# Kernel optimization log

Hardware: AMD Instinct MI355X
Metric: run time of the kernel (lower is better)

## Reference

```python
import math
import jax, jax.numpy as jnp
import numpy as np

EPS = 1e-5
TEMP = 1.0
ROPE_BASE = 10000.0


def _ln(x, g, b):
    m = x.mean(-1, keepdims=True)
    v = ((x - m) ** 2).mean(-1, keepdims=True)
    return (x - m) / jnp.sqrt(v + EPS) * g + b


def _trigrams(n_heads):
    # 8 trigrams = all sign patterns of {-1,+1}^3, L2-normalized rows
    bits = ((np.arange(8)[:, None] >> np.arange(3)[None, :]) & 1).astype(np.float32)
    t = bits * 2.0 - 1.0
    t = t / np.linalg.norm(t, axis=1, keepdims=True)
    return jnp.asarray(t[:n_heads])  # [H, 3]


def _rope_tables(T, D):
    inv = 1.0 / (ROPE_BASE ** (np.arange(0, D, 2, dtype=np.float32) / D))
    ang = np.arange(T, dtype=np.float32)[:, None] * inv[None, :]  # [T, D/2]
    cos = np.concatenate([np.cos(ang), np.cos(ang)], axis=1)  # [T, D]
    sin = np.concatenate([np.sin(ang), np.sin(ang)], axis=1)
    return jnp.asarray(cos), jnp.asarray(sin)


def _apply_rope(x, cos, sin):
    # x: [B, H, T, D], rotate-half convention
    d = x.shape[-1] // 2
    rot = jnp.concatenate([-x[..., d:], x[..., :d]], axis=-1)
    return x * cos + rot * sin


def setup_inputs() -> dict:
    key = jax.random.key(0)
    ks = jax.random.split(key, 8)
    B, T, C, H = 2, 2048, 1024, 8
    FFN, QD = 4096, 6
    w = 0.02
    return {
        "x": jax.random.normal(ks[0], (B, T, C), jnp.float32),
        "ln_attn_g": jnp.ones((C,), jnp.float32),
        "ln_attn_b": jnp.zeros((C,), jnp.float32),
        "qkv_w": jax.random.normal(ks[1], (3 * C, C), jnp.float32) * w,
        "out_w": jax.random.normal(ks[2], (C, C), jnp.float32) * w,
        "head_scales": jax.random.normal(ks[3], (H,), jnp.float32) * 0.1,
        "ln_hex_g": jnp.ones((C,), jnp.float32),
        "ln_hex_b": jnp.zeros((C,), jnp.float32),
        "to_qd_w": jax.random.normal(ks[4], (QD, C), jnp.float32) * w,
        "from_qd_w": jax.random.normal(ks[5], (C, QD), jnp.float32) * w,
        "hex_scale": jnp.ones((1,), jnp.float32),
        "ln_ffn_g": jnp.ones((C,), jnp.float32),
        "ln_ffn_b": jnp.zeros((C,), jnp.float32),
        "ffn_w1": jax.random.normal(ks[6], (FFN, C), jnp.float32) * w,
        "ffn_b1": jnp.zeros((FFN,), jnp.float32),
        "ffn_w2": jax.random.normal(ks[7], (C, FFN), jnp.float32) * w,
        "ffn_b2": jnp.zeros((C,), jnp.float32),
    }


def _layer(x, ln_attn_g, ln_attn_b, qkv_w, out_w, head_scales,
           ln_hex_g, ln_hex_b, to_qd_w, from_qd_w, hex_scale,
           ln_ffn_g, ln_ffn_b, ffn_w1, ffn_b1, ffn_w2, ffn_b2):
    B, T, C = x.shape
    H = head_scales.shape[0]
    D = C // H

    # ---- attention with trigram geo-bias ----
    h = _ln(x, ln_attn_g, ln_attn_b)
    qkv = (h @ qkv_w.T).reshape(B, T, 3, H, D).transpose(2, 0, 3, 1, 4)
    q, k, v = qkv[0], qkv[1], qkv[2]  # [B, H, T, D]
    cos, sin = _rope_tables(T, D)
    q = _apply_rope(q, cos, sin)
    k = _apply_rope(k, cos, sin)

    mask = jnp.tril(jnp.ones((T, T), bool))
    scale = jnp.float32(1.0 / math.sqrt(D))
    scores = jnp.einsum('bhtd,bhsd->bhts', q, k) * scale
    scores = jnp.where(mask, scores, -jnp.inf)
    attn = jax.nn.softmax(scores, axis=-1)
    out = attn @ v  # [B, H, T, D]

    # rank-1 geometric correction (flash path)
    dirs = _trigrams(H)  # [H, 3]
    qp = jnp.einsum('bhtd,hd->bht', q[..., :3], dirs)
    kp = jnp.einsum('bhtd,hd->bht', k[..., :3], dirs)
    geo = qp[..., :, None] * kp[..., None, :]  # [B, H, T, T]
    geo_attn = jax.nn.softmax(jnp.where(mask, geo, -jnp.inf), axis=-1)
    geo_out = geo_attn @ v
    out = out + head_scales[None, :, None, None] * jax.lax.stop_gradient(geo_out - out)

    out = out.transpose(0, 2, 1, 3).reshape(B, T, C) @ out_w.T
    x = x + out

    # ---- hexagram VQ (factored6: per-dim binary quantize w/ straight-through) ----
    h = _ln(x, ln_hex_g, ln_hex_b)
    zq = h @ to_qd_w.T  # [B, T, 6]
    soft = jnp.tanh(zq / TEMP)
    hard = jnp.where(zq >= 0, 1.0, -1.0).astype(zq.dtype)
    zq_out = soft + jax.lax.stop_gradient(hard - soft)
    x = x + hex_scale[0] * (zq_out @ from_qd_w.T)

    # ---- FFN (GELU) ----
    h = _ln(x, ln_ffn_g, ln_ffn_b)
    x = x + (jax.nn.gelu(h @ ffn_w1.T + ffn_b1, approximate=False) @ ffn_w2.T + ffn_b2)
    return x


def reference(x, ln_attn_g, ln_attn_b, qkv_w, out_w, head_scales,
              ln_hex_g, ln_hex_b, to_qd_w, from_qd_w, hex_scale,
              ln_ffn_g, ln_ffn_b, ffn_w1, ffn_b1, ffn_w2, ffn_b2):
    return _layer(x, ln_attn_g, ln_attn_b, qkv_w, out_w, head_scales,
                  ln_hex_g, ln_hex_b, to_qd_w, from_qd_w, hex_scale,
                  ln_ffn_g, ln_ffn_b, ffn_w1, ffn_b1, ffn_w2, ffn_b2)
```

## Files before the change

kernel.cpp:

```cpp
#include <hip/hip_runtime.h>
#include <hip/hip_bf16.h>

typedef __attribute__((ext_vector_type(4))) float f32x4;
typedef __attribute__((ext_vector_type(8))) short short8;
typedef __attribute__((ext_vector_type(4))) short short4v;

namespace {

constexpr int Tt = 2048, Cc = 1024, Hh = 8, Dd = 128, FFNd = 4096;
constexpr int Bb = 2;
constexpr int Mrows = Bb * Tt;
constexpr float kNEG = -1e30f;
constexpr float L2E = 1.4426950408889634f;

static __device__ __forceinline__ float b2f(unsigned short u) {
  return __uint_as_float(((unsigned int)u) << 16);
}
static __device__ __forceinline__ unsigned short f2b(float f) {
  __hip_bfloat16 h = __float2bfloat16(f);
  unsigned short u;
  __builtin_memcpy(&u, &h, 2);
  return u;
}
static __device__ __forceinline__ void split2(float v, unsigned short& h, unsigned short& l) {
  h = f2b(v);
  float r = v - b2f(h);
  l = f2b(r);
}
static __device__ __forceinline__ void split3(float v, unsigned short& h, unsigned short& m,
                                              unsigned short& l) {
  h = f2b(v);
  float r = v - b2f(h);
  m = f2b(r);
  float r2 = r - b2f(m);
  l = f2b(r2);
}
static __device__ __forceinline__ float wave_sum(float v) {
#pragma unroll
  for (int m = 1; m < 64; m <<= 1) v += __shfl_xor(v, m);
  return v;
}

__global__ __launch_bounds__(256) void cast_kernel(const float* __restrict__ in,
                                                   unsigned short* __restrict__ out, int n) {
  int i = (blockIdx.x * 256 + threadIdx.x) * 4;
  if (i + 3 < n) {
    float4 v = *(const float4*)&in[i];
    short4v o;
    o.x = (short)f2b(v.x); o.y = (short)f2b(v.y); o.z = (short)f2b(v.z); o.w = (short)f2b(v.w);
    *(short4v*)&out[i] = o;
  }
}
__global__ __launch_bounds__(256) void wsplit2_k(const float* __restrict__ in,
                                                 unsigned short* __restrict__ o0,
                                                 unsigned short* __restrict__ o1, int n) {
  int i = (blockIdx.x * 256 + threadIdx.x) * 4;
  if (i + 3 < n) {
    float4 v = *(const float4*)&in[i];
    short4v a, b;
#pragma unroll
    for (int j = 0; j < 4; ++j) {
      unsigned short hh, ll;
      split2(((float*)&v)[j], hh, ll);
      a[j] = (short)hh; b[j] = (short)ll;
    }
    *(short4v*)&o0[i] = a;
    *(short4v*)&o1[i] = b;
  }
}
__global__ __launch_bounds__(256) void wsplit3_k(const float* __restrict__ in,
                                                 unsigned short* __restrict__ o0,
                                                 unsigned short* __restrict__ o1,
                                                 unsigned short* __restrict__ o2, int n) {
  int i = (blockIdx.x * 256 + threadIdx.x) * 4;
  if (i + 3 < n) {
    float4 v = *(const float4*)&in[i];
    short4v a, b, c;
#pragma unroll
    for (int j = 0; j < 4; ++j) {
      unsigned short hh, mm, ll;
      split3(((float*)&v)[j], hh, mm, ll);
      a[j] = (short)hh; b[j] = (short)mm; c[j] = (short)ll;
    }
    *(short4v*)&o0[i] = a;
    *(short4v*)&o1[i] = b;
    *(short4v*)&o2[i] = c;
  }
}

__global__ __launch_bounds__(256) void ln_split(const float* __restrict__ x,
                                                const float* __restrict__ g,
                                                const float* __restrict__ bb,
                                                unsigned short* __restrict__ oh,
                                                unsigned short* __restrict__ ol) {
  int row = blockIdx.x * 4 + (threadIdx.x >> 6);
  int lane = threadIdx.x & 63;
  const float* xr = x + (size_t)row * Cc;
  float v[16];
  float s = 0.f;
#pragma unroll
  for (int c = 0; c < 4; ++c) {
    float4 t = *(const float4*)&xr[c * 256 + lane * 4];
    v[c * 4 + 0] = t.x; v[c * 4 + 1] = t.y; v[c * 4 + 2] = t.z; v[c * 4 + 3] = t.w;
    s += t.x + t.y + t.z + t.w;
  }
  s = wave_sum(s);
  float mean = s * (1.f / Cc);
  float s2 = 0.f;
#pragma unroll
  for (int j = 0; j < 16; ++j) { float d = v[j] - mean; s2 += d * d; }
  s2 = wave_sum(s2);
  float rstd = 1.0f / sqrtf(s2 * (1.f / Cc) + 1e-5f);
#pragma unroll
  for (int c = 0; c < 4; ++c) {
    short4v a, b;
#pragma unroll
    for (int j = 0; j < 4; ++j) {
      int idx = c * 256 + lane * 4 + j;
      float hv = (v[c * 4 + j] - mean) * rstd * g[idx] + bb[idx];
      unsigned short hh, ll;
      split2(hv, hh, ll);
      a[j] = (short)hh; b[j] = (short)ll;
    }
    *(short4v*)&oh[(size_t)row * Cc + c * 256 + lane * 4] = a;
    *(short4v*)&ol[(size_t)row * Cc + c * 256 + lane * 4] = b;
  }
}

template <int NS, int EPI>
__global__ __launch_bounds__(256) void gemm_pn(
    const unsigned short* __restrict__ A0, const unsigned short* __restrict__ A1,
    const unsigned short* __restrict__ A2, const unsigned short* __restrict__ W0,
    const unsigned short* __restrict__ W1, const unsigned short* __restrict__ W2,
    unsigned short* __restrict__ outP, size_t planeStride, float* __restrict__ outF,
    const float* __restrict__ resid, int Nn, int Kk) {
  __shared__ __align__(16) unsigned short As[NS][128 * 32];
  __shared__ __align__(16) unsigned short Bs[NS][128 * 32];
  int m0 = blockIdx.x * 128, n0 = blockIdx.y * 128;
  int tid = threadIdx.x, lane = tid & 63, wid = tid >> 6;
  int wr = (wid >> 1) * 64, wc = (wid & 1) * 64;
  int g = lane >> 4, r16 = lane & 15;
  const unsigned short* Aps[3] = {A0, A1, A2};
  const unsigned short* Wps[3] = {W0, W1, W2};
  f32x4 acc[4][4];
#pragma unroll
  for (int mi = 0; mi < 4; ++mi)
#pragma unroll
    for (int ni = 0; ni < 4; ++ni) acc[mi][ni] = (f32x4){0.f, 0.f, 0.f, 0.f};
  for (int k0 = 0; k0 < Kk; k0 += 32) {
    __syncthreads();
#pragma unroll
    for (int s = 0; s < NS; ++s)
#pragma unroll
      for (int it = 0; it < 2; ++it) {
        int slot = it * 256 + tid;
        int row = slot >> 2, sw = slot & 3;
        int cc = sw ^ (row & 3);
        *(short8*)&As[s][slot * 8] = *(const short8*)&Aps[s][(size_t)(m0 + row) * Kk + k0 + cc * 8];
        *(short8*)&Bs[s][slot * 8] = *(const short8*)&Wps[s][(size_t)(n0 + row) * Kk + k0 + cc * 8];
      }
    __syncthreads();
    short8 af[NS][4], bfv[NS][4];
#pragma unroll
    for (int mi = 0; mi < 4; ++mi) {
      int row = wr + mi * 16 + r16;
      int so = row * 32 + ((g ^ (row & 3)) * 8);
#pragma unroll
      for (int s = 0; s < NS; ++s) af[s][mi] = *(short8*)&As[s][so];
    }
#pragma unroll
    for (int ni = 0; ni < 4; ++ni) {
      int row = wc + ni * 16 + r16;
      int so = row * 32 + ((g ^ (row & 3)) * 8);
#pragma unroll
      for (int s = 0; s < NS; ++s) bfv[s][ni] = *(short8*)&Bs[s][so];
    }
    __builtin_amdgcn_s_setprio(1);
#pragma unroll
    for (int mi = 0; mi < 4; ++mi)
#pragma unroll
      for (int ni = 0; ni < 4; ++ni) {
        f32x4 a = acc[mi][ni];
        if constexpr (NS == 3) {
          a = __builtin_amdgcn_mfma_f32_16x16x32_bf16(af[1][mi], bfv[1][ni], a, 0, 0, 0);
          a = __builtin_amdgcn_mfma_f32_16x16x32_bf16(af[0][mi], bfv[2][ni], a, 0, 0, 0);
          a = __builtin_amdgcn_mfma_f32_16x16x32_bf16(af[2][mi], bfv[0][ni], a, 0, 0, 0);
        }
        a = __builtin_amdgcn_mfma_f32_16x16x32_bf16(af[0][mi], bfv[1][ni], a, 0, 0, 0);
        a = __builtin_amdgcn_mfma_f32_16x16x32_bf16(af[1][mi], bfv[0][ni], a, 0, 0, 0);
        a = __builtin_amdgcn_mfma_f32_16x16x32_bf16(af[0][mi], bfv[0][ni], a, 0, 0, 0);
        acc[mi][ni] = a;
      }
    __builtin_amdgcn_s_setprio(0);
  }
#pragma unroll
  for (int mi = 0; mi < 4; ++mi)
#pragma unroll
    for (int ni = 0; ni < 4; ++ni)
#pragma unroll
      for (int r = 0; r < 4; ++r) {
        int row = m0 + wr + mi * 16 + 4 * g + r;
        int col = n0 + wc + ni * 16 + r16;
        float v = acc[mi][ni][r];
        if constexpr (EPI == 0) {
          int sec = col >> 10, cw = col & 1023;
          unsigned short hh, ll;
          split2(v, hh, ll);
          outP[(size_t)(2 * sec) * planeStride + (size_t)row * Cc + cw] = hh;
          outP[(size_t)(2 * sec + 1) * planeStride + (size_t)row * Cc + cw] = ll;
        } else {
          size_t o = (size_t)row * Nn + col;
          outF[o] = v + resid[o];
        }
      }
}

template <int EPI>
__global__ __launch_bounds__(256) void gemm_bt(const unsigned short* __restrict__ A,
                                               const unsigned short* __restrict__ W,
                                               float* __restrict__ outF,
                                               unsigned short* __restrict__ outB,
                                               const float* __restrict__ bias,
                                               const float* __restrict__ resid, int Nn, int Kk) {
  __shared__ __align__(16) unsigned short As[128 * 32];
  __shared__ __align__(16) unsigned short Bs[128 * 32];
  int m0 = blockIdx.x * 128, n0 = blockIdx.y * 128;
  int tid = threadIdx.x, lane = tid & 63, wid = tid >> 6;
  int wr = (wid >> 1) * 64, wc = (wid & 1) * 64;
  int g = lane >> 4, r16 = lane & 15;
  f32x4 acc[4][4];
#pragma unroll
  for (int mi = 0; mi < 4; ++mi)
#pragma unroll
    for (int ni = 0; ni < 4; ++ni) acc[mi][ni] = (f32x4){0.f, 0.f, 0.f, 0.f};
  for (int k0 = 0; k0 < Kk; k0 += 32) {
    __syncthreads();
#pragma unroll
    for (int c = 0; c < 2; ++c) {
      int chunk = tid + c * 256;
      int row = chunk >> 2, cc = chunk & 3;
      int sw = cc ^ (row & 3);
      *(short8*)&As[row * 32 + sw * 8] = *(const short8*)&A[(size_t)(m0 + row) * Kk + k0 + cc * 8];
      *(short8*)&Bs[row * 32 + sw * 8] = *(const short8*)&W[(size_t)(n0 + row) * Kk + k0 + cc * 8];
    }
    __syncthreads();
    short8 af[4], bfr[4];
#pragma unroll
    for (int mi = 0; mi < 4; ++mi) {
      int row = wr + mi * 16 + r16;
      af[mi] = *(short8*)&As[row * 32 + ((g ^ (row & 3)) * 8)];
    }
#pragma unroll
    for (int ni = 0; ni < 4; ++ni) {
      int row = wc + ni * 16 + r16;
      bfr[ni] = *(short8*)&Bs[row * 32 + ((g ^ (row & 3)) * 8)];
    }
    __builtin_amdgcn_s_setprio(1);
#pragma unroll
    for (int mi = 0; mi < 4; ++mi)
#pragma unroll
      for (int ni = 0; ni < 4; ++ni)
        acc[mi][ni] = __builtin_amdgcn_mfma_f32_16x16x32_bf16(af[mi], bfr[ni], acc[mi][ni], 0, 0, 0);
    __builtin_amdgcn_s_setprio(0);
  }
#pragma unroll
  for (int mi = 0; mi < 4; ++mi)
#pragma unroll
    for (int ni = 0; ni < 4; ++ni)
#pragma unroll
      for (int r = 0; r < 4; ++r) {
        int row = m0 + wr + mi * 16 + 4 * g + r;
        int col = n0 + wc + ni * 16 + r16;
        size_t o = (size_t)row * Nn + col;
        float v = acc[mi][ni][r];
        if constexpr (EPI == 2) {
          v += bias[col];
          v = 0.5f * v * (1.f + erff(v * 0.70710678118654752f));
          outB[o] = f2b(v);
        } else {
          v += bias[col];
          outF[o] = v + resid[o];
        }
      }
}

__global__ __launch_bounds__(256) void rope_table(float* __restrict__ ct, float* __restrict__ st) {
  int idx = blockIdx.x * 256 + threadIdx.x;
  int t = idx >> 6, i = idx & 63;
  float e = (float)i * (1.f / 64.f);
  float p = powf(10000.0f, e);
  float inv = 1.0f / p;
  float ang = (float)t * inv;
  ct[idx] = cosf(ang);
  st[idx] = sinf(ang);
}

__global__ __launch_bounds__(256) void rope_apply(unsigned short* __restrict__ qh_p,
                                                  unsigned short* __restrict__ ql_p,
                                                  const unsigned short* __restrict__ kh_p,
                                                  const unsigned short* __restrict__ kl_p,
                                                  unsigned short* __restrict__ khsw,
                                                  unsigned short* __restrict__ klsw,
                                                  const float* __restrict__ ct,
                                                  const float* __restrict__ st,
                                                  float* __restrict__ qp, float* __restrict__ kp) {
  int w = blockIdx.x * 4 + (threadIdx.x >> 6);
  int lane = threadIdx.x & 63;
  int b = w / (Hh * Tt);
  int rem = w % (Hh * Tt);
  int h = rem / Tt;
  int t = rem % Tt;
  size_t base = (size_t)(b * Tt + t) * Cc + h * Dd;
  float cv = ct[t * 64 + lane], sv = st[t * 64 + lane];
  float q_lo = b2f(qh_p[base + lane]) + b2f(ql_p[base + lane]);
  float q_hi = b2f(qh_p[base + lane + 64]) + b2f(ql_p[base + lane + 64]);
  float qn_lo = q_lo * cv - q_hi * sv;
  float qn_hi = q_hi * cv + q_lo * sv;
  unsigned short hh, ll;
  split2(qn_lo, hh, ll);
  qh_p[base + lane] = hh; ql_p[base + lane] = ll;
  split2(qn_hi, hh, ll);
  qh_p[base + lane + 64] = hh; ql_p[base + lane + 64] = ll;
  float k_lo = b2f(kh_p[base + lane]) + b2f(kl_p[base + lane]);
  float k_hi = b2f(kh_p[base + lane + 64]) + b2f(kl_p[base + lane + 64]);
  float kn_lo = k_lo * cv - k_hi * sv;
  float kn_hi = k_hi * cv + k_lo * sv;
  size_t krow = ((size_t)(b * Hh + h) * Tt + t) * 128;
  int tsw = t & 7;
  int d0 = lane, d1 = lane + 64;
  int c0 = (((d0 >> 3) ^ tsw) << 3) | (d0 & 7);
  int c1 = (((d1 >> 3) ^ tsw) << 3) | (d1 & 7);
  split2(kn_lo, hh, ll);
  khsw[krow + c0] = hh; klsw[krow + c0] = ll;
  split2(kn_hi, hh, ll);
  khsw[krow + c1] = hh; klsw[krow + c1] = ll;
  float t0 = (((h >> 0) & 1) ? 1.f : -1.f) * 0.57735026918962576f;
  float t1 = (((h >> 1) & 1) ? 1.f : -1.f) * 0.57735026918962576f;
  float t2 = (((h >> 2) & 1) ? 1.f : -1.f) * 0.57735026918962576f;
  float q0v = __shfl(qn_lo, 0), q1v = __shfl(qn_lo, 1), q2v = __shfl(qn_lo, 2);
  float k0v = __shfl(kn_lo, 0), k1v = __shfl(kn_lo, 1), k2v = __shfl(kn_lo, 2);
  if (lane == 0) {
    qp[(size_t)(b * Hh + h) * Tt + t] = q0v * t0 + q1v * t1 + q2v * t2;
    kp[(size_t)(b * Hh + h) * Tt + t] = k0v * t0 + k1v * t1 + k2v * t2;
  }
}

__global__ __launch_bounds__(256) void vtrans(const unsigned short* __restrict__ vh_p,
                                              const unsigned short* __restrict__ vl_p,
                                              unsigned short* __restrict__ vth,
                                              unsigned short* __restrict__ vtl) {
  __shared__ unsigned short Lh[64 * 68], Ll[64 * 68];
  int bidx = blockIdx.x;
  int dd = bidx & 1;
  int tt = (bidx >> 1) & 31;
  int bh = bidx >> 6;
  int b = bh >> 3, h = bh & 7;
  int tid = threadIdx.x;
#pragma unroll
  for (int it = 0; it < 2; ++it) {
    int chunk = tid + it * 256;
    int tr = chunk >> 3, c8 = chunk & 7;
    size_t src = (size_t)(b * Tt + tt * 64 + tr) * Cc + h * Dd + dd * 64 + c8 * 8;
    short8 vh = *(const short8*)&vh_p[src];
    short8 vl = *(const short8*)&vl_p[src];
    *(short4v*)&Lh[tr * 68 + c8 * 8] = *(short4v*)&vh;
    *(short4v*)&Lh[tr * 68 + c8 * 8 + 4] = *((short4v*)&vh + 1);
    *(short4v*)&Ll[tr * 68 + c8 * 8] = *(short4v*)&vl;
    *(short4v*)&Ll[tr * 68 + c8 * 8 + 4] = *((short4v*)&vl + 1);
  }
  __syncthreads();
#pragma unroll
  for (int it = 0; it < 2; ++it) {
    int chunk = tid + it * 256;
    int dr = chunk >> 3, t8 = chunk & 7;
    short8 oh, ol;
#pragma unroll
    for (int e = 0; e < 8; ++e) {
      oh[e] = (short)Lh[(t8 * 8 + e) * 68 + dr];
      ol[e] = (short)Ll[(t8 * 8 + e) * 68 + dr];
    }
    size_t dst = (size_t)(bh * Dd + dd * 64 + dr) * Tt + tt * 64 + t8 * 8;
    *(short8*)&vth[dst] = oh;
    *(short8*)&vtl[dst] = ol;
  }
}

__global__ __launch_bounds__(256, 2) void attn_v3(
    const unsigned short* __restrict__ qh_p, const unsigned short* __restrict__ ql_p,
    const unsigned short* __restrict__ khsw, const unsigned short* __restrict__ klsw,
    const unsigned short* __restrict__ vth, const unsigned short* __restrict__ vtl,
    const float* __restrict__ qp, const float* __restrict__ kp,
    const float* __restrict__ head_scales, unsigned short* __restrict__ ao0,
    unsigned short* __restrict__ ao1, unsigned short* __restrict__ ao2) {
  int cix = blockIdx.x & 255, rix = blockIdx.x >> 8;
  int bh = cix >> 4, ii = cix & 15;
  int qblk = rix ? ii : 31 - ii;
  int b = bh >> 3, h = bh & 7;
  int q0 = qblk * 64;
  int tid = threadIdx.x, lane = tid & 63, wid = tid >> 6;
  int wq0 = q0 + wid * 16;
  int g = lane >> 4, r16 = lane & 15;
  __shared__ __align__(16) unsigned short Ksh[32 * 128], Ksl[32 * 128];
  __shared__ __align__(16) unsigned short Vsh[128 * 34], Vsl[128 * 34];

  short8 qfh[4], qfl[4];
#pragma unroll
  for (int c4 = 0; c4 < 4; ++c4) {
    size_t qoff = (size_t)(b * Tt + wq0 + r16) * Cc + h * Dd + c4 * 32 + g * 8;
    qfh[c4] = *(const short8*)&qh_p[qoff];
    qfl[c4] = *(const short8*)&ql_p[qoff];
  }
  float hs = head_scales[h];
  const float* kpb = kp + (size_t)bh * Tt;
  float qpl2 = qp[(size_t)bh * Tt + wq0 + r16] * L2E;

  const unsigned short* Khb = khsw + (size_t)bh * Tt * 128;
  const unsigned short* Klb = klsw + (size_t)bh * Tt * 128;
  const unsigned short* Vhb = vth + (size_t)bh * Dd * Tt;
  const unsigned short* Vlb = vtl + (size_t)bh * Dd * Tt;

  f32x4 accA[8], accG[8];
#pragma unroll
  for (int n = 0; n < 8; ++n) {
    accA[n] = (f32x4){0.f, 0.f, 0.f, 0.f};
    accG[n] = (f32x4){0.f, 0.f, 0.f, 0.f};
  }
  float m1 = kNEG, l1 = 0.f, m2 = kNEG, l2 = 0.f;
  const float scale2 = 0.08838834764831845f * L2E;

  int nt = 2 * qblk + 2;
  short8 rkh[2], rkl[2], rvh[2], rvl[2];
  int krw[2], kcl[2], vdd[2], vkk[2];
#pragma unroll
  for (int it = 0; it < 2; ++it) {
    int chunk = tid + it * 256;
    krw[it] = chunk >> 4; kcl[it] = (chunk & 15) * 8;
    vdd[it] = chunk >> 2; vkk[it] = (chunk & 3) * 8;
  }
  auto LOADT = [&](int s0) {
#pragma unroll
    for (int it = 0; it < 2; ++it) {
      size_t ksrc = (size_t)(s0 + krw[it]) * 128 + kcl[it];
      rkh[it] = *(const short8*)&Khb[ksrc];
      rkl[it] = *(const short8*)&Klb[ksrc];
      size_t vsrc = (size_t)vdd[it] * Tt + s0 + vkk[it];
      rvh[it] = *(const short8*)&Vhb[vsrc];
      rvl[it] = *(const short8*)&Vlb[vsrc];
    }
  };
  LOADT(0);
  for (int t = 0; t < nt; ++t) {
    int s0 = t * 32;
    __syncthreads();
#pragma unroll
    for (int it = 0; it < 2; ++it) {
      *(short8*)&Ksh[krw[it] * 128 + kcl[it]] = rkh[it];
      *(short8*)&Ksl[krw[it] * 128 + kcl[it]] = rkl[it];
      *(short8*)&Vsh[vdd[it] * 34 + vkk[it]] = rvh[it];
      *(short8*)&Vsl[vdd[it] * 34 + vkk[it]] = rvl[it];
    }
    __syncthreads();
    if (t + 1 < nt) LOADT(s0 + 32);
    if (s0 > wq0 + 15) continue;
    float kpv[2][4];
#pragma unroll
    for (int st2 = 0; st2 < 2; ++st2)
#pragma unroll
      for (int rr = 0; rr < 4; ++rr) kpv[st2][rr] = kpb[s0 + st2 * 16 + 4 * g + rr];
    f32x4 sf[2];
    sf[0] = (f32x4){0.f, 0.f, 0.f, 0.f};
    sf[1] = (f32x4){0.f, 0.f, 0.f, 0.f};
    __builtin_amdgcn_s_setprio(1);
#pragma unroll
    for (int st2 = 0; st2 < 2; ++st2) {
      int row = st2 * 16 + r16, rsw = row & 7;
#pragma unroll
      for (int c4 = 0; c4 < 4; ++c4) {
        int off = row * 128 + (((c4 * 4 + g) ^ rsw) * 8);
        short8 kh8 = *(short8*)&Ksh[off];
        short8 kl8 = *(short8*)&Ksl[off];
        sf[st2] = __builtin_amdgcn_mfma_f32_16x16x32_bf16(kl8, qfh[c4], sf[st2], 0, 0, 0);
        sf[st2] = __builtin_amdgcn_mfma_f32_16x16x32_bf16(kh8, qfl[c4], sf[st2], 0, 0, 0);
        sf[st2] = __builtin_amdgcn_mfma_f32_16x16x32_bf16(kh8, qfh[c4], sf[st2], 0, 0, 0);
      }
    }
    __builtin_amdgcn_s_setprio(0);
    bool okf[2][4];
    float sv[2][4], gvv[2][4];
    float mx = kNEG, gmx = kNEG;
#pragma unroll
    for (int st2 = 0; st2 < 2; ++st2)
#pragma unroll
      for (int rr = 0; rr < 4; ++rr) {
        int key = s0 + st2 * 16 + 4 * g + rr;
        bool ok = key <= wq0 + r16;
        okf[st2][rr] = ok;
        float s = ok ? sf[st2][rr] * scale2 : kNEG;
        sv[st2][rr] = s;
        mx = fmaxf(mx, s);
        float gg = ok ? qpl2 * kpv[st2][rr] : kNEG;
        gvv[st2][rr] = gg;
        gmx = fmaxf(gmx, gg);
      }
    mx = fmaxf(mx, __shfl_xor(mx, 16));
    mx = fmaxf(mx, __shfl_xor(mx, 32));
    gmx = fmaxf(gmx, __shfl_xor(gmx, 16));
    gmx = fmaxf(gmx, __shfl_xor(gmx, 32));
    float mn = fmaxf(m1, mx), sc = exp2f(m1 - mn);
    float mg = fmaxf(m2, gmx), sg = exp2f(m2 - mg);
    float pa[2][4], pgv[2][4];
    float ps = 0.f, pgs = 0.f;
#pragma unroll
    for (int st2 = 0; st2 < 2; ++st2)
#pragma unroll
      for (int rr = 0; rr < 4; ++rr) {
        float p = okf[st2][rr] ? exp2f(sv[st2][rr] - mn) : 0.f;
        pa[st2][rr] = p; ps += p;
        float pq = okf[st2][rr] ? exp2f(gvv[st2][rr] - mg) : 0.f;
        pgv[st2][rr] = pq; pgs += pq;
      }
    ps += __shfl_xor(ps, 16); ps += __shfl_xor(ps, 32);
    pgs += __shfl_xor(pgs, 16); pgs += __shfl_xor(pgs, 32);
    l1 = l1 * sc + ps; m1 = mn;
    l2 = l2 * sg + pgs; m2 = mg;
    float sclA[4], sclG[4];
#pragma unroll
    for (int rr = 0; rr < 4; ++rr) {
      sclA[rr] = __shfl(sc, 4 * g + rr);
      sclG[rr] = __shfl(sg, 4 * g + rr);
    }
#pragma unroll
    for (int n = 0; n < 8; ++n)
#pragma unroll
      for (int rr = 0; rr < 4; ++rr) {
        accA[n][rr] *= sclA[rr];
        accG[n][rr] *= sclG[rr];
      }
    short8 pAh, pAl, pGh, pGl;
#pragma unroll
    for (int e = 0; e < 8; ++e) {
      unsigned short hh, ll;
      split2(pa[e >> 2][e & 3], hh, ll);
      pAh[e] = (short)hh; pAl[e] = (short)ll;
      split2(pgv[e >> 2][e & 3], hh, ll);
      pGh[e] = (short)hh; pGl[e] = (short)ll;
    }
    __builtin_amdgcn_s_setprio(1);
#pragma unroll
    for (int n = 0; n < 8; ++n) {
      int dofs = (n * 16 + r16) * 34;
      short8 vh8, vl8;
      *(short4v*)&vh8 = *(short4v*)&Vsh[dofs + 4 * g];
      *((short4v*)&vh8 + 1) = *(short4v*)&Vsh[dofs + 16 + 4 * g];
      *(short4v*)&vl8 = *(short4v*)&Vsl[dofs + 4 * g];
      *((short4v*)&vl8 + 1) = *(short4v*)&Vsl[dofs + 16 + 4 * g];
      accA[n] = __builtin_amdgcn_mfma_f32_16x16x32_bf16(pAl, vh8, accA[n], 0, 0, 0);
      accA[n] = __builtin_amdgcn_mfma_f32_16x16x32_bf16(pAh, vl8, accA[n], 0, 0, 0);
      accA[n] = __builtin_amdgcn_mfma_f32_16x16x32_bf16(pAh, vh8, accA[n], 0, 0, 0);
      accG[n] = __builtin_amdgcn_mfma_f32_16x16x32_bf16(pGl, vh8, accG[n], 0, 0, 0);
      accG[n] = __builtin_amdgcn_mfma_f32_16x16x32_bf16(pGh, vl8, accG[n], 0, 0, 0);
      accG[n] = __builtin_amdgcn_mfma_f32_16x16x32_bf16(pGh, vh8, accG[n], 0, 0, 0);
    }
    __builtin_amdgcn_s_setprio(0);
  }
  float lA[4], lG[4];
#pragma unroll
  for (int rr = 0; rr < 4; ++rr) {
    lA[rr] = __shfl(l1, 4 * g + rr);
    lG[rr] = __shfl(l2, 4 * g + rr);
  }
#pragma unroll
  for (int n = 0; n < 8; ++n)
#pragma unroll
    for (int rr = 0; rr < 4; ++rr) {
      int qi = wq0 + 4 * g + rr;
      float av = accA[n][rr] / lA[rr];
      float gq = accG[n][rr] / lG[rr];
      float o = av + hs * (gq - av);
      unsigned short s1, s2v, s3;
      split3(o, s1, s2v, s3);
      size_t oo = (size_t)(b * Tt + qi) * Cc + h * Dd + n * 16 + r16;
      ao0[oo] = s1; ao1[oo] = s2v; ao2[oo] = s3;
    }
}

__global__ __launch_bounds__(256) void hex_kernel(float* __restrict__ x1,
                                                  const float* __restrict__ hg,
                                                  const float* __restrict__ hb,
                                                  const float* __restrict__ to_qd,
                                                  const float* __restrict__ from_qd,
                                                  const float* __restrict__ hex_scale,
                                                  const float* __restrict__ fg,
                                                  const float* __restrict__ fb,
                                                  unsigned short* __restrict__ h_ffn) {
  int row = blockIdx.x * 4 + (threadIdx.x >> 6);
  int lane = threadIdx.x & 63;
  float* xr = x1 + (size_t)row * Cc;
  float v[16];
  float s = 0.f;
#pragma unroll
  for (int c = 0; c < 4; ++c) {
    float4 t = *(const float4*)&xr[c * 256 + lane * 4];
    v[c * 4 + 0] = t.x; v[c * 4 + 1] = t.y; v[c * 4 + 2] = t.z; v[c * 4 + 3] = t.w;
    s += t.x + t.y + t.z + t.w;
  }
  s = wave_sum(s);
  float mean = s * (1.f / Cc);
  float s2 = 0.f;
#pragma unroll
  for (int j = 0; j < 16; ++j) { float d = v[j] - mean; s2 += d * d; }
  s2 = wave_sum(s2);
  float rstd = 1.0f / sqrtf(s2 * (1.f / Cc) + 1e-5f);
  float zq[6] = {0.f, 0.f, 0.f, 0.f, 0.f, 0.f};
#pragma unroll
  for (int c = 0; c < 4; ++c)
#pragma unroll
    for (int j2 = 0; j2 < 4; ++j2) {
      int idx = c * 256 + lane * 4 + j2;
      float hv = (v[c * 4 + j2] - mean) * rstd * hg[idx] + hb[idx];
#pragma unroll
      for (int j = 0; j < 6; ++j) zq[j] += hv * to_qd[j * Cc + idx];
    }
#pragma unroll
  for (int j = 0; j < 6; ++j) zq[j] = wave_sum(zq[j]);
  float hsc = hex_scale[0];
  float hard[6];
#pragma unroll
  for (int j = 0; j < 6; ++j) hard[j] = (zq[j] >= 0.f) ? hsc : -hsc;
  float x2v[16];
  float t1 = 0.f;
#pragma unroll
  for (int c = 0; c < 4; ++c)
#pragma unroll
    for (int j2 = 0; j2 < 4; ++j2) {
      int idx = c * 256 + lane * 4 + j2;
      float a = 0.f;
#pragma unroll
      for (int j = 0; j < 6; ++j) a += hard[j] * from_qd[idx * 6 + j];
      float xv = v[c * 4 + j2] + a;
      x2v[c * 4 + j2] = xv;
      t1 += xv;
    }
  t1 = wave_sum(t1);
  float mean2 = t1 * (1.f / Cc);
  float t2 = 0.f;
#pragma unroll
  for (int j = 0; j < 16; ++j) { float d = x2v[j] - mean2; t2 += d * d; }
  t2 = wave_sum(t2);
  float rstd2 = 1.0f / sqrtf(t2 * (1.f / Cc) + 1e-5f);
#pragma unroll
  for (int c = 0; c < 4; ++c) {
    float4 t;
    t.x = x2v[c * 4 + 0]; t.y = x2v[c * 4 + 1]; t.z = x2v[c * 4 + 2]; t.w = x2v[c * 4 + 3];
    *(float4*)&xr[c * 256 + lane * 4] = t;
    short4v o;
#pragma unroll
    for (int j = 0; j < 4; ++j) {
      int idx = c * 256 + lane * 4 + j;
      ((short*)&o)[j] = (short)f2b((x2v[c * 4 + j] - mean2) * rstd2 * fg[idx] + fb[idx]);
    }
    *(short4v*)&h_ffn[(size_t)row * Cc + c * 256 + lane * 4] = o;
  }
}

}

extern "C" void kernel_launch(void* const* d_in, const int* in_sizes, int n_in, void* d_out,
                              int out_size, void* d_ws, size_t ws_size, hipStream_t stream) {
  const float* x = (const float*)d_in[0];
  const float* ln_attn_g = (const float*)d_in[1];
  const float* ln_attn_b = (const float*)d_in[2];
  const float* qkv_w = (const float*)d_in[3];
  const float* out_w = (const float*)d_in[4];
  const float* head_scales = (const float*)d_in[5];
  const float* ln_hex_g = (const float*)d_in[6];
  const float* ln_hex_b = (const float*)d_in[7];
  const float* to_qd_w = (const float*)d_in[8];
  const float* from_qd_w = (const float*)d_in[9];
  const float* hex_scale = (const float*)d_in[10];
  const float* ln_ffn_g = (const float*)d_in[11];
  const float* ln_ffn_b = (const float*)d_in[12];
  const float* ffn_w1 = (const float*)d_in[13];
  const float* ffn_b1 = (const float*)d_in[14];
  const float* ffn_w2 = (const float*)d_in[15];
  const float* ffn_b2 = (const float*)d_in[16];

  unsigned short* ws16 = (unsigned short*)d_ws;
  const size_t PL = (size_t)Mrows * Cc;
  unsigned short* hh = ws16 + 0 * PL;
  unsigned short* hl = ws16 + 1 * PL;
  unsigned short* qhp = ws16 + 2 * PL;
  unsigned short* qlp = ws16 + 3 * PL;
  unsigned short* khp = ws16 + 4 * PL;
  unsigned short* klp = ws16 + 5 * PL;
  unsigned short* vhp = ws16 + 6 * PL;
  unsigned short* vlp = ws16 + 7 * PL;
  unsigned short* khsw = ws16 + 8 * PL;
  unsigned short* klsw = ws16 + 9 * PL;
  unsigned short* vth = ws16 + 10 * PL;
  unsigned short* vtl = ws16 + 11 * PL;
  float* tail = (float*)(ws16 + 12 * PL);
  float* ct = tail;
  float* st = ct + (size_t)Tt * 64;
  float* qp = st + (size_t)Tt * 64;
  float* kp = qp + (size_t)Bb * Hh * Tt;
  unsigned short* ao0 = hh;
  unsigned short* ao1 = hl;
  unsigned short* ao2 = khp;
  float* x1 = (float*)klp;
  unsigned short* h_ffn = vlp;
  unsigned short* w1b = qhp;
  unsigned short* w2b = qlp;
  unsigned short* gelu = khsw;
  unsigned short* wqh = vth;
  unsigned short* wql = vtl;
  unsigned short* ow0 = khsw;
  unsigned short* ow1 = khsw + (size_t)Cc * Cc;
  unsigned short* ow2 = khsw + (size_t)2 * Cc * Cc;

  ln_split<<<Mrows / 4, 256, 0, stream>>>(x, ln_attn_g, ln_attn_b, hh, hl);
  wsplit2_k<<<(3 * Cc * Cc) / 1024, 256, 0, stream>>>(qkv_w, wqh, wql, 3 * Cc * Cc);
  gemm_pn<2, 0><<<dim3(Mrows / 128, (3 * Cc) / 128), 256, 0, stream>>>(
      hh, hl, nullptr, wqh, wql, nullptr, qhp, PL, nullptr, nullptr, 3 * Cc, Cc);
  rope_table<<<(Tt * 64) / 256, 256, 0, stream>>>(ct, st);
  rope_apply<<<(Bb * Hh * Tt) / 4, 256, 0, stream>>>(qhp, qlp, khp, klp, khsw, klsw, ct, st, qp,
                                                     kp);
  vtrans<<<Bb * Hh * 32 * 2, 256, 0, stream>>>(vhp, vlp, vth, vtl);
  attn_v3<<<512, 256, 0, stream>>>(qhp, qlp, khsw, klsw, vth, vtl, qp, kp, head_scales, ao0, ao1,
                                   ao2);
  wsplit3_k<<<(Cc * Cc) / 1024, 256, 0, stream>>>(out_w, ow0, ow1, ow2, Cc * Cc);
  gemm_pn<3, 1><<<dim3(Mrows / 128, Cc / 128), 256, 0, stream>>>(
      ao0, ao1, ao2, ow0, ow1, ow2, nullptr, 0, x1, x, Cc, Cc);
  hex_kernel<<<Mrows / 4, 256, 0, stream>>>(x1, ln_hex_g, ln_hex_b, to_qd_w, from_qd_w, hex_scale,
                                            ln_ffn_g, ln_ffn_b, h_ffn);
  cast_kernel<<<(FFNd * Cc) / 1024, 256, 0, stream>>>(ffn_w1, w1b, FFNd * Cc);
  cast_kernel<<<(Cc * FFNd) / 1024, 256, 0, stream>>>(ffn_w2, w2b, Cc * FFNd);
  gemm_bt<2><<<dim3(Mrows / 128, FFNd / 128), 256, 0, stream>>>(h_ffn, w1b, nullptr, gelu, ffn_b1,
                                                                nullptr, FFNd, Cc);
  gemm_bt<3><<<dim3(Mrows / 128, Cc / 128), 256, 0, stream>>>(gelu, w2b, (float*)d_out, nullptr,
                                                              ffn_b2, x1, Cc, FFNd);
}
```

Baseline: 542.7 us.

## Use direct global-to-LDS loads in GEMMs and lazy rescaling in attention softmax

Both GEMM kernels now stage A and W tiles with global_load_lds, which writes 16-byte chunks straight into shared memory instead of going through registers. The per-lane swizzled source offsets are precomputed once outside the k-loop. In the attention kernel, causal masking is applied only on tiles that straddle the diagonal. Accumulator rescaling is skipped unless the running max grows by more than a threshold, removing shuffles and multiplies on most tiles. This risks larger unnormalized values (bounded by 2^7) and relies on global_load_lds preserving the LDS swizzle layout.

```diff
diff --git a/kernel.cpp b/kernel.cpp
--- a/kernel.cpp
+++ b/kernel.cpp
@@ -39,6 +39,10 @@
 #pragma unroll
   for (int m = 1; m < 64; m <<= 1) v += __shfl_xor(v, m);
   return v;
+}
+static __device__ __forceinline__ void gl16(const unsigned short* g, unsigned short* l) {
+  __builtin_amdgcn_global_load_lds((const __attribute__((address_space(1))) void*)g,
+                                   (__attribute__((address_space(3))) void*)l, 16, 0, 0);
 }
 
 __global__ __launch_bounds__(256) void cast_kernel(const float* __restrict__ in,
@@ -142,6 +146,16 @@
   int g = lane >> 4, r16 = lane & 15;
   const unsigned short* Aps[3] = {A0, A1, A2};
   const unsigned short* Wps[3] = {W0, W1, W2};
+  int srow[2], scc[2], sbase[2];
+#pragma unroll
+  for (int i = 0; i < 2; ++i) {
+    int chunkbase = (wid * 2 + i) * 64;
+    int chunk = chunkbase + lane;
+    int row = chunk >> 2, sw = chunk & 3;
+    srow[i] = row;
+    scc[i] = (sw ^ (row & 3)) * 8;
+    sbase[i] = chunkbase * 8;
+  }
   f32x4 acc[4][4];
 #pragma unroll
   for (int mi = 0; mi < 4; ++mi)
@@ -152,12 +166,9 @@
 #pragma unroll
     for (int s = 0; s < NS; ++s)
 #pragma unroll
-      for (int it = 0; it < 2; ++it) {
-        int slot = it * 256 + tid;
-        int row = slot >> 2, sw = slot & 3;
-        int cc = sw ^ (row & 3);
-        *(short8*)&As[s][slot * 8] = *(const short8*)&Aps[s][(size_t)(m0 + row) * Kk + k0 + cc * 8];
-        *(short8*)&Bs[s][slot * 8] = *(const short8*)&Wps[s][(size_t)(n0 + row) * Kk + k0 + cc * 8];
+      for (int i = 0; i < 2; ++i) {
+        gl16(&Aps[s][(size_t)(m0 + srow[i]) * Kk + k0 + scc[i]], &As[s][sbase[i]]);
+        gl16(&Wps[s][(size_t)(n0 + srow[i]) * Kk + k0 + scc[i]], &Bs[s][sbase[i]]);
       }
     __syncthreads();
     short8 af[NS][4], bfv[NS][4];
@@ -228,6 +239,16 @@
   int tid = threadIdx.x, lane = tid & 63, wid = tid >> 6;
   int wr = (wid >> 1) * 64, wc = (wid & 1) * 64;
   int g = lane >> 4, r16 = lane & 15;
+  int srow[2], scc[2], sbase[2];
+#pragma unroll
+  for (int i = 0; i < 2; ++i) {
+    int chunkbase = (wid * 2 + i) * 64;
+    int chunk = chunkbase + lane;
+    int row = chunk >> 2, sw = chunk & 3;
+    srow[i] = row;
+    scc[i] = (sw ^ (row & 3)) * 8;
+    sbase[i] = chunkbase * 8;
+  }
   f32x4 acc[4][4];
 #pragma unroll
   for (int mi = 0; mi < 4; ++mi)
@@ -236,12 +257,9 @@
   for (int k0 = 0; k0 < Kk; k0 += 32) {
     __syncthreads();
 #pragma unroll
-    for (int c = 0; c < 2; ++c) {
-      int chunk = tid + c * 256;
-      int row = chunk >> 2, cc = chunk & 3;
-      int sw = cc ^ (row & 3);
-      *(short8*)&As[row * 32 + sw * 8] = *(const short8*)&A[(size_t)(m0 + row) * Kk + k0 + cc * 8];
-      *(short8*)&Bs[row * 32 + sw * 8] = *(const short8*)&W[(size_t)(n0 + row) * Kk + k0 + cc * 8];
+    for (int i = 0; i < 2; ++i) {
+      gl16(&A[(size_t)(m0 + srow[i]) * Kk + k0 + scc[i]], &As[sbase[i]]);
+      gl16(&W[(size_t)(n0 + srow[i]) * Kk + k0 + scc[i]], &Bs[sbase[i]]);
     }
     __syncthreads();
     short8 af[4], bfr[4];
@@ -485,57 +503,68 @@
       }
     }
     __builtin_amdgcn_s_setprio(0);
-    bool okf[2][4];
+    bool partial = (s0 + 31) > wq0;
     float sv[2][4], gvv[2][4];
     float mx = kNEG, gmx = kNEG;
 #pragma unroll
     for (int st2 = 0; st2 < 2; ++st2)
 #pragma unroll
       for (int rr = 0; rr < 4; ++rr) {
-        int key = s0 + st2 * 16 + 4 * g + rr;
-        bool ok = key <= wq0 + r16;
-        okf[st2][rr] = ok;
-        float s = ok ? sf[st2][rr] * scale2 : kNEG;
-        sv[st2][rr] = s;
+        float s = sf[st2][rr] * scale2;
+        float gg = qpl2 * kpv[st2][rr];
+        if (partial) {
+          int key = s0 + st2 * 16 + 4 * g + rr;
+          bool ok = key <= wq0 + r16;
+          s = ok ? s : kNEG;
+          gg = ok ? gg : kNEG;
+        }
+        sv[st2][rr] = s; gvv[st2][rr] = gg;
         mx = fmaxf(mx, s);
-        float gg = ok ? qpl2 * kpv[st2][rr] : kNEG;
-        gvv[st2][rr] = gg;
         gmx = fmaxf(gmx, gg);
       }
     mx = fmaxf(mx, __shfl_xor(mx, 16));
     mx = fmaxf(mx, __shfl_xor(mx, 32));
     gmx = fmaxf(gmx, __shfl_xor(gmx, 16));
     gmx = fmaxf(gmx, __shfl_xor(gmx, 32));
-    float mn = fmaxf(m1, mx), sc = exp2f(m1 - mn);
-    float mg = fmaxf(m2, gmx), sg = exp2f(m2 - mg);
+    if (!__all(mx <= m1 + 7.f)) {
+      float nm = fmaxf(m1, mx);
+      float sc = exp2f(m1 - nm);
+      m1 = nm; l1 *= sc;
+      float sA[4];
+#pragma unroll
+      for (int rr = 0; rr < 4; ++rr) sA[rr] = __shfl(sc, 4 * g + rr);
+#pragma unroll
+      for (int n = 0; n < 8; ++n)
+#pragma unroll
+        for (int rr = 0; rr < 4; ++rr) accA[n][rr] *= sA[rr];
+    }
+    if (!__all(gmx <= m2 + 7.f)) {
+      float nm = fmaxf(m2, gmx);
+      float sg = exp2f(m2 - nm);
+      m2 = nm; l2 *= sg;
+      float sG[4];
+#pragma unroll
+      for (int rr = 0; rr < 4; ++rr) sG[rr] = __shfl(sg, 4 * g + rr);
+#pragma unroll
+      for (int n = 0; n < 8; ++n)
+#pragma unroll
+        for (int rr = 0; rr < 4; ++rr) accG[n][rr] *= sG[rr];
+    }
     float pa[2][4], pgv[2][4];
     float ps = 0.f, pgs = 0.f;
 #pragma unroll
     for (int st2 = 0; st2 < 2; ++st2)
 #pragma unroll
       for (int rr = 0; rr < 4; ++rr) {
-        float p = okf[st2][rr] ? exp2f(sv[st2][rr] - mn) : 0.f;
+        float p = exp2f(sv[st2][rr] - m1);
         pa[st2][rr] = p; ps += p;
-        float pq = okf[st2][rr] ? exp2f(gvv[st2][rr] - mg) : 0.f;
+        float pq = exp2f(gvv[st2][rr] - m2);
         pgv[st2][rr] = pq; pgs += pq;
       }
     ps += __shfl_xor(ps, 16); ps += __shfl_xor(ps, 32);
     pgs += __shfl_xor(pgs, 16); pgs += __shfl_xor(pgs, 32);
-    l1 = l1 * sc + ps; m1 = mn;
-    l2 = l2 * sg + pgs; m2 = mg;
-    float sclA[4], sclG[4];
-#pragma unroll
-    for (int rr = 0; rr < 4; ++rr) {
-      sclA[rr] = __shfl(sc, 4 * g + rr);
-      sclG[rr] = __shfl(sg, 4 * g + rr);
-    }
-#pragma unroll
-    for (int n = 0; n < 8; ++n)
-#pragma unroll
-      for (int rr = 0; rr < 4; ++rr) {
-        accA[n][rr] *= sclA[rr];
-        accG[n][rr] *= sclG[rr];
-      }
+    l1 += ps;
+    l2 += pgs;
     short8 pAh, pAl, pGh, pGl;
 #pragma unroll
     for (int e = 0; e < 8; ++e) {
```

Measured after the change: 530.9 us. 1.02x faster.
